# Kernel tuning notes

Hardware: AMD Instinct MI355X
Metric: run time of the kernel (lower is better)

## Reference

```python
import jax, jax.numpy as jnp
import numpy as np

NUM_HEADS = 32
NUM_KV_HEADS = 8
HEAD_DIM = 128
NEG_INF = -1e9


def rotate_half(x):
    x1, x2 = jnp.split(x, 2, axis=-1)
    return jnp.concatenate([-x2, x1], axis=-1)


def setup_inputs() -> dict:
    key = jax.random.key(0)
    ks = jax.random.split(key, 8)
    B, S, H = 2, 2048, 4096
    hidden_states = jax.random.normal(ks[0], (B, S, H), jnp.float32) * 0.02
    # additive causal mask [1,1,S,S]: 0 on/below diagonal, -1e9 above
    causal = jnp.tril(jnp.ones((S, S), bool))
    attention_mask = jnp.where(causal, 0.0, NEG_INF)[None, None, :, :].astype(jnp.float32)
    # RoPE tables (theta=500000 style), shape [1,S,head_dim]
    inv_freq = 1.0 / (500000.0 ** (np.arange(0, HEAD_DIM, 2, dtype=np.float32) / HEAD_DIM))
    t = np.arange(S, dtype=np.float32)
    freqs = np.outer(t, inv_freq)  # [S, head_dim/2]
    emb = np.concatenate([freqs, freqs], axis=-1)  # [S, head_dim]
    cos = jnp.asarray(np.cos(emb))[None]
    sin = jnp.asarray(np.sin(emb))[None]
    scale = 0.02
    wq = jax.random.normal(ks[1], (NUM_HEADS * HEAD_DIM, H), jnp.float32) * scale
    wk = jax.random.normal(ks[2], (NUM_KV_HEADS * HEAD_DIM, H), jnp.float32) * scale
    wv = jax.random.normal(ks[3], (NUM_KV_HEADS * HEAD_DIM, H), jnp.float32) * scale
    wo = jax.random.normal(ks[4], (H, NUM_HEADS * HEAD_DIM), jnp.float32) * scale
    return {"hidden_states": hidden_states, "attention_mask": attention_mask,
            "cos": cos, "sin": sin, "wq": wq, "wk": wk, "wv": wv, "wo": wo}


def reference(hidden_states, attention_mask, cos, sin, wq, wk, wv, wo):
    B, S, H = hidden_states.shape
    nh, nkv, hd = NUM_HEADS, NUM_KV_HEADS, HEAD_DIM
    groups = nh // nkv
    # QKV projections (bias=False)
    q = jnp.einsum('bsh,dh->bsd', hidden_states, wq).reshape(B, S, nh, hd).transpose(0, 2, 1, 3)
    k = jnp.einsum('bsh,dh->bsd', hidden_states, wk).reshape(B, S, nkv, hd).transpose(0, 2, 1, 3)
    v = jnp.einsum('bsh,dh->bsd', hidden_states, wv).reshape(B, S, nkv, hd).transpose(0, 2, 1, 3)
    # RoPE: cos/sin [1,S,hd] -> broadcast over head dim [1,1,S,hd]
    c = cos[:, None, :, :]
    s = sin[:, None, :, :]
    q = q * c + rotate_half(q) * s
    k = k * c + rotate_half(k) * s
    # GQA: repeat_kv
    k = jnp.repeat(k, groups, axis=1)  # [B,nh,S,hd]
    v = jnp.repeat(v, groups, axis=1)
    # SDPA with additive mask
    scores = jnp.einsum('bhqd,bhkd->bhqk', q, k) / jnp.sqrt(jnp.float32(hd))
    scores = scores + attention_mask[:, :, :, :k.shape[2]]
    attn = jax.nn.softmax(scores, axis=-1)
    out = jnp.einsum('bhqk,bhkd->bhqd', attn, v)  # [B,nh,S,hd]
    out = out.transpose(0, 2, 1, 3).reshape(B, S, nh * hd)
    return jnp.einsum('bsd,hd->bsh', out, wo)
```

## Files before the change

### kernel.cpp

```cpp
#include <hip/hip_runtime.h>
#include <hip/hip_bf16.h>

typedef __attribute__((ext_vector_type(8))) __bf16 bf16x8;
typedef __attribute__((ext_vector_type(4))) float f32x4;
typedef __attribute__((ext_vector_type(16))) float f32x16;
typedef __attribute__((ext_vector_type(4))) unsigned int u32x4;

#define SEQ 2048
#define NH 32
#define NKV 8
#define HD 128

__device__ __forceinline__ ushort f2bf(float f) {
  unsigned u = __builtin_bit_cast(unsigned, f);
  unsigned r = (u + 0x7fffu + ((u >> 16) & 1u)) >> 16;
  return (ushort)r;
}
__device__ __forceinline__ float bf2f(ushort h) {
  return __builtin_bit_cast(float, ((unsigned)h) << 16);
}
__device__ __forceinline__ unsigned cvt_pk_bf16(float lo, float hi) {
  unsigned r;
  asm("v_cvt_pk_bf16_f32 %0, %1, %2" : "=v"(r) : "v"(lo), "v"(hi));
  return r;
}
__device__ __forceinline__ void gload16(const void* g, void* l) {
  __builtin_amdgcn_global_load_lds(
      (const __attribute__((address_space(1))) void*)g,
      (__attribute__((address_space(3))) void*)l, 16, 0, 0);
}

__global__ __launch_bounds__(256) void f2bf_kernel(const float4* __restrict__ in,
                                                   ushort4* __restrict__ out, int n4) {
  int i = blockIdx.x * 256 + threadIdx.x;
  if (i >= n4) return;
  float4 v = in[i];
  ushort4 o;
  o.x = f2bf(v.x); o.y = f2bf(v.y); o.z = f2bf(v.z); o.w = f2bf(v.w);
  out[i] = o;
}

template <int OUTF32>
__global__ __launch_bounds__(256) void gemm_bt_kernel(const ushort* __restrict__ A,
                                                      const ushort* __restrict__ B,
                                                      void* __restrict__ C,
                                                      int M, int N, int K) {
  __shared__ ushort As[2][128 * 32];
  __shared__ ushort Bs[2][128 * 32];
  const int tid = threadIdx.x;
  const int w = tid >> 6, l = tid & 63;
  const int lr = l & 15, lc = l >> 4;
  const int bx = blockIdx.x, by = blockIdx.y;
  const int wr = w >> 1, wc = w & 1;

  f32x4 z = {0.f, 0.f, 0.f, 0.f};
  f32x4 acc[4][4];
#pragma unroll
  for (int i = 0; i < 4; ++i)
#pragma unroll
    for (int j = 0; j < 4; ++j) acc[i][j] = z;

  const ushort* aSrc = A + (size_t)(by * 128 + 32 * w + (l >> 2)) * K + (l & 3) * 8;
  const ushort* bSrc = B + (size_t)(bx * 128 + 32 * w + (l >> 2)) * K + (l & 3) * 8;
  const int ldsOff = (32 * w) * 32;

#pragma unroll
  for (int q = 0; q < 2; ++q) {
    gload16(aSrc + (size_t)q * 16 * K, &As[0][ldsOff + q * 512]);
    gload16(bSrc + (size_t)q * 16 * K, &Bs[0][ldsOff + q * 512]);
  }
  __syncthreads();

  const int nk = K >> 5;
  int cur = 0;
  for (int kt = 0; kt < nk; ++kt) {
    if (kt + 1 < nk) {
      const ushort* a2 = aSrc + (size_t)(kt + 1) * 32;
      const ushort* b2 = bSrc + (size_t)(kt + 1) * 32;
#pragma unroll
      for (int q = 0; q < 2; ++q) {
        gload16(a2 + (size_t)q * 16 * K, &As[cur ^ 1][ldsOff + q * 512]);
        gload16(b2 + (size_t)q * 16 * K, &Bs[cur ^ 1][ldsOff + q * 512]);
      }
    }
    bf16x8 af[4], bfr[4];
#pragma unroll
    for (int i = 0; i < 4; ++i)
      af[i] = *(const bf16x8*)&As[cur][(64 * wr + 16 * i + lr) * 32 + lc * 8];
#pragma unroll
    for (int j = 0; j < 4; ++j)
      bfr[j] = *(const bf16x8*)&Bs[cur][(64 * wc + 16 * j + lr) * 32 + lc * 8];
#pragma unroll
    for (int i = 0; i < 4; ++i)
#pragma unroll
      for (int j = 0; j < 4; ++j)
        acc[i][j] = __builtin_amdgcn_mfma_f32_16x16x32_bf16(af[i], bfr[j], acc[i][j], 0, 0, 0);
    __syncthreads();
    cur ^= 1;
  }

#pragma unroll
  for (int i = 0; i < 4; ++i)
#pragma unroll
    for (int j = 0; j < 4; ++j) {
      int row = by * 128 + 64 * wr + 16 * i + lc * 4;
      int col = bx * 128 + 64 * wc + 16 * j + lr;
#pragma unroll
      for (int r = 0; r < 4; ++r) {
        if (OUTF32)
          ((float*)C)[(size_t)(row + r) * N + col] = acc[i][j][r];
        else
          ((ushort*)C)[(size_t)(row + r) * N + col] = f2bf(acc[i][j][r]);
      }
    }
}

template <int OUTF32>
__global__ __launch_bounds__(512, 2) void gemm256_kernel(const ushort* __restrict__ A,
                                                         const ushort* __restrict__ B,
                                                         void* __restrict__ C,
                                                         int M, int N, int K) {
  __shared__ ushort As[2][256 * 64];
  __shared__ ushort Bs[2][256 * 64];
  const int tid = threadIdx.x;
  const int w = tid >> 6, l = tid & 63;
  const int lr = l & 15, lc = l >> 4;
  const int wr = w >> 2, wc = w & 3;

  const int nbx = N >> 8;
  const int cpx = gridDim.x >> 3;
  const int sw = (blockIdx.x & 7) * cpx + (blockIdx.x >> 3);
  const int bx = sw % nbx, by = sw / nbx;

  const ushort* Asrc = A + (size_t)(by * 256) * K;
  const ushort* Bsrc = B + (size_t)(bx * 256) * K;

  f32x4 z = {0.f, 0.f, 0.f, 0.f};
  f32x4 acc[8][4];
#pragma unroll
  for (int m = 0; m < 8; ++m)
#pragma unroll
    for (int n = 0; n < 4; ++n) acc[m][n] = z;

  const int NK = K >> 6;

  auto stage = [&](int kt2, int s) {
    if (kt2 >= NK) return;
    const int mat = s >> 1, half = s & 1;
    const ushort* g = mat ? Bsrc : Asrc;
    char* lb = (char*)(mat ? &Bs[kt2 & 1][0] : &As[kt2 & 1][0]) + half * 16384 + w * 1024;
#pragma unroll
    for (int i = 0; i < 2; ++i) {
      int row = half * 128 + i * 64 + w * 8 + (l >> 3);
      int csw = ((l & 7) * 16) ^ ((row & 7) << 4);
      gload16(g + (size_t)row * K + kt2 * 64 + (csw >> 1), lb + i * 8192);
    }
  };

  stage(0, 0); stage(0, 1); stage(0, 2); stage(0, 3);
  stage(1, 0);

  bf16x8 af[4][2], bfr[4][2];
  for (int kt = 0; kt < NK; ++kt) {
    const char* Ab = (const char*)&As[kt & 1][0];
    const char* Bb = (const char*)&Bs[kt & 1][0];
    if (kt + 1 < NK) asm volatile("s_waitcnt vmcnt(2)" ::: "memory");
    else             asm volatile("s_waitcnt vmcnt(0)" ::: "memory");
    asm volatile("s_barrier" ::: "memory");

#pragma unroll
    for (int m = 0; m < 4; ++m) {
      int row = wr * 128 + m * 16 + lr;
#pragma unroll
      for (int ks = 0; ks < 2; ++ks)
        af[m][ks] = *(const bf16x8*)(Ab + row * 128 + ((ks * 64 + lc * 16) ^ ((row & 7) << 4)));
    }
#pragma unroll
    for (int n = 0; n < 2; ++n) {
      int row = wc * 64 + n * 16 + lr;
#pragma unroll
      for (int ks = 0; ks < 2; ++ks)
        bfr[n][ks] = *(const bf16x8*)(Bb + row * 128 + ((ks * 64 + lc * 16) ^ ((row & 7) << 4)));
    }
    stage(kt + 1, 1);
    __builtin_amdgcn_s_setprio(1);
#pragma unroll
    for (int m = 0; m < 4; ++m)
#pragma unroll
      for (int n = 0; n < 2; ++n)
#pragma unroll
        for (int ks = 0; ks < 2; ++ks)
          acc[m][n] = __builtin_amdgcn_mfma_f32_16x16x32_bf16(af[m][ks], bfr[n][ks], acc[m][n], 0, 0, 0);
    __builtin_amdgcn_s_setprio(0);
    asm volatile("s_barrier" ::: "memory");

#pragma unroll
    for (int n = 2; n < 4; ++n) {
      int row = wc * 64 + n * 16 + lr;
#pragma unroll
      for (int ks = 0; ks < 2; ++ks)
        bfr[n][ks] = *(const bf16x8*)(Bb + row * 128 + ((ks * 64 + lc * 16) ^ ((row & 7) << 4)));
    }
    stage(kt + 1, 2);
    __builtin_amdgcn_s_setprio(1);
#pragma unroll
    for (int m = 0; m < 4; ++m)
#pragma unroll
      for (int n = 2; n < 4; ++n)
#pragma unroll
        for (int ks = 0; ks < 2; ++ks)
          acc[m][n] = __builtin_amdgcn_mfma_f32_16x16x32_bf16(af[m][ks], bfr[n][ks], acc[m][n], 0, 0, 0);
    __builtin_amdgcn_s_setprio(0);
    asm volatile("s_barrier" ::: "memory");

#pragma unroll
    for (int m = 0; m < 4; ++m) {
      int row = wr * 128 + (m + 4) * 16 + lr;
#pragma unroll
      for (int ks = 0; ks < 2; ++ks)
        af[m][ks] = *(const bf16x8*)(Ab + row * 128 + ((ks * 64 + lc * 16) ^ ((row & 7) << 4)));
    }
    stage(kt + 1, 3);
    __builtin_amdgcn_s_setprio(1);
#pragma unroll
    for (int m = 0; m < 4; ++m)
#pragma unroll
      for (int n = 0; n < 2; ++n)
#pragma unroll
        for (int ks = 0; ks < 2; ++ks)
          acc[m + 4][n] = __builtin_amdgcn_mfma_f32_16x16x32_bf16(af[m][ks], bfr[n][ks], acc[m + 4][n], 0, 0, 0);
    __builtin_amdgcn_s_setprio(0);
    asm volatile("s_barrier" ::: "memory");

    stage(kt + 2, 0);
    __builtin_amdgcn_s_setprio(1);
#pragma unroll
    for (int m = 0; m < 4; ++m)
#pragma unroll
      for (int n = 2; n < 4; ++n)
#pragma unroll
        for (int ks = 0; ks < 2; ++ks)
          acc[m + 4][n] = __builtin_amdgcn_mfma_f32_16x16x32_bf16(af[m][ks], bfr[n][ks], acc[m + 4][n], 0, 0, 0);
    __builtin_amdgcn_s_setprio(0);
  }

#pragma unroll
  for (int m = 0; m < 8; ++m)
#pragma unroll
    for (int n = 0; n < 4; ++n) {
      int row = by * 256 + wr * 128 + m * 16 + lc * 4;
      int col = bx * 256 + wc * 64 + n * 16 + lr;
#pragma unroll
      for (int r = 0; r < 4; ++r) {
        if (OUTF32)
          ((float*)C)[(size_t)(row + r) * N + col] = acc[m][n][r];
        else
          ((ushort*)C)[(size_t)(row + r) * N + col] = f2bf(acc[m][n][r]);
      }
    }
}

__global__ __launch_bounds__(256) void rope_kernel(const ushort* __restrict__ in,
                                                   const float* __restrict__ cosb,
                                                   const float* __restrict__ sinb,
                                                   ushort* __restrict__ out,
                                                   int hshift, float scale) {
  int idx = blockIdx.x * 256 + threadIdx.x;
  int d = idx & 63;
  int nh = 1 << hshift;
  int h = (idx >> 6) & (nh - 1);
  int rowg = idx >> (6 + hshift);
  int s = rowg & (SEQ - 1);
  int b = rowg >> 11;
  const ushort* p = in + (size_t)rowg * (nh * HD) + h * HD + d;
  float x = bf2f(p[0]), y = bf2f(p[64]);
  float c = cosb[s * HD + d], sn = sinb[s * HD + d];
  ushort* qo = out + (((size_t)(b * nh + h)) * SEQ + s) * HD + d;
  qo[0] = f2bf((x * c - y * sn) * scale);
  qo[64] = f2bf((y * c + x * sn) * scale);
}

__global__ __launch_bounds__(256) void vtrans_kernel(const ushort* __restrict__ vin,
                                                     ushort* __restrict__ vout) {
  __shared__ ushort t[64][66];
  const int s0 = blockIdx.x * 64;
  const int c0 = blockIdx.y * 64;
  const int b = blockIdx.z;
  const int tx = threadIdx.x & 63;
  const int ty = threadIdx.x >> 6;
#pragma unroll
  for (int rr = 0; rr < 64; rr += 4) {
    int r = rr + ty;
    t[r][tx] = vin[((size_t)(b * SEQ + s0 + r)) * (NKV * HD) + c0 + tx];
  }
  __syncthreads();
#pragma unroll
  for (int rr = 0; rr < 64; rr += 4) {
    int c = rr + ty;
    int cg = c0 + c;
    int kvh = cg >> 7, d = cg & 127;
    vout[(((size_t)(b * NKV + kvh)) * HD + d) * SEQ + s0 + tx] = t[tx][c];
  }
}

__global__ __launch_bounds__(256, 2) void attn_kernel(const ushort* __restrict__ Qh,
                                                      const ushort* __restrict__ Kh,
                                                      const ushort* __restrict__ Vt,
                                                      ushort* __restrict__ Out) {
  __shared__ ushort Kl[2][64 * 128];

  const int tid = threadIdx.x;
  const int w = tid >> 6, l = tid & 63;
  const int lq = l & 31;
  const int hl = l >> 5;

  const int n = blockIdx.x;
  const int m = ((n & 7) << 6) + (n >> 3);
  const int pp = m >> 5;
  const int rm = m & 31;
  const int h2 = rm >> 3;
  const int qpi = rm & 7;
  const int bb = pp >> 3, kvh = pp & 7;
  const int hh = kvh * 4 + h2;
  const int bh = bb * 32 + hh;

  const ushort* Kbase = Kh + ((size_t)(bb * NKV + kvh) * SEQ) * HD;
  const ushort* Vbase = Vt + ((size_t)(bb * NKV + kvh) * HD) * SEQ;

  auto stageK = [&](int buf, int t) {
    const int kv0 = t * 64;
#pragma unroll
    for (int q = 0; q < 4; ++q) {
      int chunk = 4 * w + q;
      int row = chunk * 4 + (l >> 4);
      int cs = ((l & 15) ^ (row & 7)) * 8;
      gload16(Kbase + ((size_t)(kv0 + row)) * HD + cs, &Kl[buf][chunk * 512]);
    }
  };

  for (int qsel = 0; qsel < 2; ++qsel) {
    const int qt = qsel ? (15 - qpi) : qpi;
    const int q0 = qt * 128;
    const int wrow0 = q0 + 32 * w;
    const int qrow = wrow0 + lq;

    bf16x8 qf[8];
    {
      const ushort* qrp = Qh + ((size_t)bh * SEQ + qrow) * HD + 8 * hl;
#pragma unroll
      for (int s8 = 0; s8 < 8; ++s8) qf[s8] = *(const bf16x8*)(qrp + 16 * s8);
    }

    f32x16 o[4];
#pragma unroll
    for (int db = 0; db < 4; ++db)
#pragma unroll
      for (int i = 0; i < 16; ++i) o[db][i] = 0.f;
    float m_run = -1e30f, l_run = 0.f;

    const int ntw = 2 * qt + (w >> 1) + 1;
    const int ntb = 2 * qt + 2;

    stageK(0, 0);
    __syncthreads();

    int cur = 0;
    for (int t = 0; t < ntb; ++t) {
      const int kv0 = t * 64;
      if (t + 1 < ntb) stageK(cur ^ 1, t + 1);

      if (t < ntw) {
        f32x16 sacc[2];
#pragma unroll
        for (int b2 = 0; b2 < 2; ++b2)
#pragma unroll
          for (int i = 0; i < 16; ++i) sacc[b2][i] = 0.f;

        const int swz = lq & 7;
        __builtin_amdgcn_s_setprio(1);
#pragma unroll
        for (int s8 = 0; s8 < 8; ++s8) {
#pragma unroll
          for (int b2 = 0; b2 < 2; ++b2) {
            int row = 32 * b2 + lq;
            bf16x8 kf = *(const bf16x8*)((const char*)&Kl[cur][0] + row * 256 +
                                         (((2 * s8 + hl) ^ swz) << 4));
            sacc[b2] = __builtin_amdgcn_mfma_f32_32x32x16_bf16(kf, qf[s8], sacc[b2], 0, 0, 0);
          }
        }
        __builtin_amdgcn_s_setprio(0);

        if (t == ntw - 1) {
#pragma unroll
          for (int b2 = 0; b2 < 2; ++b2)
#pragma unroll
            for (int r = 0; r < 16; ++r) {
              int kv = kv0 + 32 * b2 + (r & 3) + 8 * (r >> 2) + 4 * hl;
              if (kv > qrow) sacc[b2][r] = -1e30f;
            }
        }

        float mx = sacc[0][0];
#pragma unroll
        for (int r = 1; r < 16; ++r) mx = fmaxf(mx, sacc[0][r]);
#pragma unroll
        for (int r = 0; r < 16; ++r) mx = fmaxf(mx, sacc[1][r]);
        mx = fmaxf(mx, __shfl_xor(mx, 32));

        if (__any(mx > m_run + 8.0f)) {
          float mn = fmaxf(m_run, mx);
          float sc = __expf(m_run - mn);
          m_run = mn;
          l_run *= sc;
#pragma unroll
          for (int db = 0; db < 4; ++db) o[db] *= sc;
        }

        float sum = 0.f;
#pragma unroll
        for (int b2 = 0; b2 < 2; ++b2)
#pragma unroll
          for (int r = 0; r < 16; ++r) {
            float e = __expf(sacc[b2][r] - m_run);
            sacc[b2][r] = e;
            sum += e;
          }
        sum += __shfl_xor(sum, 32);
        l_run += sum;

        unsigned pw[2][8];
#pragma unroll
        for (int b2 = 0; b2 < 2; ++b2)
#pragma unroll
          for (int i = 0; i < 8; ++i)
            pw[b2][i] = cvt_pk_bf16(sacc[b2][2 * i], sacc[b2][2 * i + 1]);

#pragma unroll
        for (int s = 0; s < 4; ++s) {
          const int b2 = s >> 1, bs = 4 * (s & 1);
          unsigned wA = pw[b2][bs], wB = pw[b2][bs + 1], wC = pw[b2][bs + 2], wD = pw[b2][bs + 3];
          unsigned s1 = hl ? wA : wC, s2 = hl ? wB : wD;
          unsigned rx1 = (unsigned)__shfl_xor((int)s1, 32);
          unsigned rx2 = (unsigned)__shfl_xor((int)s2, 32);
          u32x4 fw = {hl ? rx1 : wA, hl ? rx2 : wB, hl ? wC : rx1, hl ? wD : rx2};
          bf16x8 pfrag = __builtin_bit_cast(bf16x8, fw);
          const ushort* vp = Vbase + (size_t)lq * SEQ + kv0 + 16 * s + 8 * hl;
          bf16x8 vf[4];
#pragma unroll
          for (int db = 0; db < 4; ++db) vf[db] = *(const bf16x8*)(vp + (size_t)(32 * db) * SEQ);
          __builtin_amdgcn_s_setprio(1);
#pragma unroll
          for (int db = 0; db < 4; ++db)
            o[db] = __builtin_amdgcn_mfma_f32_32x32x16_bf16(vf[db], pfrag, o[db], 0, 0, 0);
          __builtin_amdgcn_s_setprio(0);
        }
      }
      __syncthreads();
      cur ^= 1;
    }

    const float inv = 1.0f / l_run;
    ushort* outp = Out + ((size_t)bb * SEQ + qrow) * (NH * HD) + hh * HD;
#pragma unroll
    for (int db = 0; db < 4; ++db)
#pragma unroll
      for (int i = 0; i < 8; ++i) {
        unsigned wrd = cvt_pk_bf16(o[db][2 * i] * inv, o[db][2 * i + 1] * inv);
        int d = 32 * db + 2 * (i & 1) + 8 * (i >> 1) + 4 * hl;
        *(unsigned*)(outp + d) = wrd;
      }
  }
}

extern "C" void kernel_launch(void* const* d_in, const int* in_sizes, int n_in,
                              void* d_out, int out_size, void* d_ws, size_t ws_size,
                              hipStream_t stream) {
  const float* hs = (const float*)d_in[0];
  const float* cosb = (const float*)d_in[2];
  const float* sinb = (const float*)d_in[3];
  const float* wq = (const float*)d_in[4];
  const float* wk = (const float*)d_in[5];
  const float* wv = (const float*)d_in[6];
  const float* wo = (const float*)d_in[7];

  char* ws = (char*)d_ws;
  ushort* hs_bf = (ushort*)(ws);
  ushort* wq_bf = (ushort*)(ws + 33554432);
  ushort* wk_bf = (ushort*)(ws + 67108864);
  ushort* wv_bf = (ushort*)(ws + 75497472);
  ushort* wo_bf = (ushort*)(ws + 83886080);
  ushort* q_lin = (ushort*)(ws + 117440512);
  ushort* k_lin = (ushort*)(ws + 150994944);
  ushort* v_lin = (ushort*)(ws + 159383552);
  ushort* Qh = hs_bf;
  ushort* Kh = wq_bf;
  ushort* Vt = (ushort*)(ws + 41943040);
  ushort* attn_out = q_lin;

  f2bf_kernel<<<16384, 256, 0, stream>>>((const float4*)hs, (ushort4*)hs_bf, 4194304);
  f2bf_kernel<<<16384, 256, 0, stream>>>((const float4*)wq, (ushort4*)wq_bf, 4194304);
  f2bf_kernel<<<4096, 256, 0, stream>>>((const float4*)wk, (ushort4*)wk_bf, 1048576);
  f2bf_kernel<<<4096, 256, 0, stream>>>((const float4*)wv, (ushort4*)wv_bf, 1048576);
  f2bf_kernel<<<16384, 256, 0, stream>>>((const float4*)wo, (ushort4*)wo_bf, 4194304);

  gemm256_kernel<0><<<256, 512, 0, stream>>>(hs_bf, wq_bf, q_lin, 4096, 4096, 4096);
  gemm_bt_kernel<0><<<dim3(8, 32), 256, 0, stream>>>(hs_bf, wk_bf, k_lin, 4096, 1024, 4096);
  gemm_bt_kernel<0><<<dim3(8, 32), 256, 0, stream>>>(hs_bf, wv_bf, v_lin, 4096, 1024, 4096);

  rope_kernel<<<32768, 256, 0, stream>>>(q_lin, cosb, sinb, Qh, 5, 0.08838834764831845f);
  rope_kernel<<<8192, 256, 0, stream>>>(k_lin, cosb, sinb, Kh, 3, 1.0f);
  vtrans_kernel<<<dim3(32, 16, 2), 256, 0, stream>>>(v_lin, Vt);

  attn_kernel<<<512, 256, 0, stream>>>(Qh, Kh, Vt, attn_out);

  gemm256_kernel<1><<<256, 512, 0, stream>>>(attn_out, wo_bf, d_out, 4096, 4096, 4096);
}
```

Measured before the change: 622.3 us.

## Split attention into per-q-tile blocks, fuse K/V GEMM, use exp2 softmax

The attention kernel now gives each block a single 128-row query tile, heaviest tiles first, and launches 1024 blocks instead of 512 blocks that each processed two paired tiles. Occupancy is raised to 4 blocks per CU via launch bounds. The K and V projections become one GEMM over the contiguous wk/wv weights, writing into a single interleaved buffer that rope and the V transpose read with a new stride. Softmax uses the raw v_exp_f32 (base 2) with log2(e) folded into the Q scale, and the max and sum reductions become tree reductions. The higher occupancy target caps registers per thread and risks spills, and per-block Q loads and K staging setup are now repeated more often.

```diff
diff --git a/kernel.cpp b/kernel.cpp
--- a/kernel.cpp
+++ b/kernel.cpp
@@ -22,6 +22,11 @@
 __device__ __forceinline__ unsigned cvt_pk_bf16(float lo, float hi) {
   unsigned r;
   asm("v_cvt_pk_bf16_f32 %0, %1, %2" : "=v"(r) : "v"(lo), "v"(hi));
+  return r;
+}
+__device__ __forceinline__ float exp2_fast(float x) {
+  float r;
+  asm("v_exp_f32 %0, %1" : "=v"(r) : "v"(x));
   return r;
 }
 __device__ __forceinline__ void gload16(const void* g, void* l) {
@@ -260,7 +265,7 @@
     }
 }
 
-__global__ __launch_bounds__(256) void rope_kernel(const ushort* __restrict__ in,
+__global__ __launch_bounds__(256) void rope_kernel(const ushort* __restrict__ in, int ld,
                                                    const float* __restrict__ cosb,
                                                    const float* __restrict__ sinb,
                                                    ushort* __restrict__ out,
@@ -272,7 +277,7 @@
   int rowg = idx >> (6 + hshift);
   int s = rowg & (SEQ - 1);
   int b = rowg >> 11;
-  const ushort* p = in + (size_t)rowg * (nh * HD) + h * HD + d;
+  const ushort* p = in + (size_t)rowg * ld + h * HD + d;
   float x = bf2f(p[0]), y = bf2f(p[64]);
   float c = cosb[s * HD + d], sn = sinb[s * HD + d];
   ushort* qo = out + (((size_t)(b * nh + h)) * SEQ + s) * HD + d;
@@ -291,7 +296,7 @@
 #pragma unroll
   for (int rr = 0; rr < 64; rr += 4) {
     int r = rr + ty;
-    t[r][tx] = vin[((size_t)(b * SEQ + s0 + r)) * (NKV * HD) + c0 + tx];
+    t[r][tx] = vin[((size_t)(b * SEQ + s0 + r)) * 2048 + 1024 + c0 + tx];
   }
   __syncthreads();
 #pragma unroll
@@ -303,7 +308,7 @@
   }
 }
 
-__global__ __launch_bounds__(256, 2) void attn_kernel(const ushort* __restrict__ Qh,
+__global__ __launch_bounds__(256, 4) void attn_kernel(const ushort* __restrict__ Qh,
                                                       const ushort* __restrict__ Kh,
                                                       const ushort* __restrict__ Vt,
                                                       ushort* __restrict__ Out) {
@@ -315,17 +320,37 @@
   const int hl = l >> 5;
 
   const int n = blockIdx.x;
-  const int m = ((n & 7) << 6) + (n >> 3);
-  const int pp = m >> 5;
-  const int rm = m & 31;
-  const int h2 = rm >> 3;
-  const int qpi = rm & 7;
+  const int xcd = n & 7, i = n >> 3;
+  const int qt = 15 - (i >> 3);
+  const int j = i & 7;
+  const int pp = 2 * xcd + (j >> 2);
+  const int h2 = j & 3;
   const int bb = pp >> 3, kvh = pp & 7;
   const int hh = kvh * 4 + h2;
   const int bh = bb * 32 + hh;
+  const int q0 = qt * 128;
+  const int wrow0 = q0 + 32 * w;
+  const int qrow = wrow0 + lq;
 
   const ushort* Kbase = Kh + ((size_t)(bb * NKV + kvh) * SEQ) * HD;
   const ushort* Vbase = Vt + ((size_t)(bb * NKV + kvh) * HD) * SEQ;
+
+  bf16x8 qf[8];
+  {
+    const ushort* qrp = Qh + ((size_t)bh * SEQ + qrow) * HD + 8 * hl;
+#pragma unroll
+    for (int s8 = 0; s8 < 8; ++s8) qf[s8] = *(const bf16x8*)(qrp + 16 * s8);
+  }
+
+  f32x16 o[4];
+#pragma unroll
+  for (int db = 0; db < 4; ++db)
+#pragma unroll
+    for (int i2 = 0; i2 < 16; ++i2) o[db][i2] = 0.f;
+  float m_run = -1e30f, l_run = 0.f;
+
+  const int ntw = 2 * qt + (w >> 1) + 1;
+  const int ntb = 2 * qt + 2;
 
   auto stageK = [&](int buf, int t) {
     const int kv0 = t * 64;
@@ -338,138 +363,120 @@
     }
   };
 
-  for (int qsel = 0; qsel < 2; ++qsel) {
-    const int qt = qsel ? (15 - qpi) : qpi;
-    const int q0 = qt * 128;
-    const int wrow0 = q0 + 32 * w;
-    const int qrow = wrow0 + lq;
-
-    bf16x8 qf[8];
-    {
-      const ushort* qrp = Qh + ((size_t)bh * SEQ + qrow) * HD + 8 * hl;
-#pragma unroll
-      for (int s8 = 0; s8 < 8; ++s8) qf[s8] = *(const bf16x8*)(qrp + 16 * s8);
-    }
-
-    f32x16 o[4];
-#pragma unroll
-    for (int db = 0; db < 4; ++db)
-#pragma unroll
-      for (int i = 0; i < 16; ++i) o[db][i] = 0.f;
-    float m_run = -1e30f, l_run = 0.f;
-
-    const int ntw = 2 * qt + (w >> 1) + 1;
-    const int ntb = 2 * qt + 2;
-
-    stageK(0, 0);
+  stageK(0, 0);
+  __syncthreads();
+
+  int cur = 0;
+  for (int t = 0; t < ntb; ++t) {
+    const int kv0 = t * 64;
+    if (t + 1 < ntb) stageK(cur ^ 1, t + 1);
+
+    if (t < ntw) {
+      f32x16 sacc[2];
+#pragma unroll
+      for (int b2 = 0; b2 < 2; ++b2)
+#pragma unroll
+        for (int i2 = 0; i2 < 16; ++i2) sacc[b2][i2] = 0.f;
+
+      const int swz = lq & 7;
+      __builtin_amdgcn_s_setprio(1);
+#pragma unroll
+      for (int s8 = 0; s8 < 8; ++s8) {
+#pragma unroll
+        for (int b2 = 0; b2 < 2; ++b2) {
+          int row = 32 * b2 + lq;
+          bf16x8 kf = *(const bf16x8*)((const char*)&Kl[cur][0] + row * 256 +
+                                       (((2 * s8 + hl) ^ swz) << 4));
+          sacc[b2] = __builtin_amdgcn_mfma_f32_32x32x16_bf16(kf, qf[s8], sacc[b2], 0, 0, 0);
+        }
+      }
+      __builtin_amdgcn_s_setprio(0);
+
+      if (t == ntw - 1) {
+#pragma unroll
+        for (int b2 = 0; b2 < 2; ++b2)
+#pragma unroll
+          for (int r = 0; r < 16; ++r) {
+            int kv = kv0 + 32 * b2 + (r & 3) + 8 * (r >> 2) + 4 * hl;
+            if (kv > qrow) sacc[b2][r] = -1e30f;
+          }
+      }
+
+      float tm[8];
+#pragma unroll
+      for (int r = 0; r < 8; ++r)
+        tm[r] = fmaxf(fmaxf(sacc[0][r], sacc[0][r + 8]),
+                      fmaxf(sacc[1][r], sacc[1][r + 8]));
+#pragma unroll
+      for (int s2 = 4; s2; s2 >>= 1)
+#pragma unroll
+        for (int r = 0; r < s2; ++r) tm[r] = fmaxf(tm[r], tm[r + s2]);
+      float mx = fmaxf(tm[0], __shfl_xor(tm[0], 32));
+
+      if (__any(mx > m_run + 8.0f)) {
+        float mn = fmaxf(m_run, mx);
+        float sc = exp2_fast(m_run - mn);
+        m_run = mn;
+        l_run *= sc;
+#pragma unroll
+        for (int db = 0; db < 4; ++db) o[db] *= sc;
+      }
+
+#pragma unroll
+      for (int b2 = 0; b2 < 2; ++b2)
+#pragma unroll
+        for (int r = 0; r < 16; ++r) sacc[b2][r] = exp2_fast(sacc[b2][r] - m_run);
+      float ts[8];
+#pragma unroll
+      for (int r = 0; r < 8; ++r)
+        ts[r] = (sacc[0][r] + sacc[0][r + 8]) + (sacc[1][r] + sacc[1][r + 8]);
+#pragma unroll
+      for (int s2 = 4; s2; s2 >>= 1)
+#pragma unroll
+        for (int r = 0; r < s2; ++r) ts[r] += ts[r + s2];
+      l_run += ts[0] + __shfl_xor(ts[0], 32);
+
+      unsigned pw[2][8];
+#pragma unroll
+      for (int b2 = 0; b2 < 2; ++b2)
+#pragma unroll
+        for (int i2 = 0; i2 < 8; ++i2)
+          pw[b2][i2] = cvt_pk_bf16(sacc[b2][2 * i2], sacc[b2][2 * i2 + 1]);
+
+#pragma unroll
+      for (int s = 0; s < 4; ++s) {
+        const int b2 = s >> 1, bs = 4 * (s & 1);
+        unsigned wA = pw[b2][bs], wB = pw[b2][bs + 1], wC = pw[b2][bs + 2], wD = pw[b2][bs + 3];
+        unsigned s1 = hl ? wA : wC, s2v = hl ? wB : wD;
+        unsigned rx1 = (unsigned)__shfl_xor((int)s1, 32);
+        unsigned rx2 = (unsigned)__shfl_xor((int)s2v, 32);
+        u32x4 fw = {hl ? rx1 : wA, hl ? rx2 : wB, hl ? wC : rx1, hl ? wD : rx2};
+        bf16x8 pfrag = __builtin_bit_cast(bf16x8, fw);
+        const ushort* vp = Vbase + (size_t)lq * SEQ + kv0 + 16 * s + 8 * hl;
+        bf16x8 vf[4];
+#pragma unroll
+        for (int db = 0; db < 4; ++db) vf[db] = *(const bf16x8*)(vp + (size_t)(32 * db) * SEQ);
+        __builtin_amdgcn_s_setprio(1);
+#pragma unroll
+        for (int db = 0; db < 4; ++db)
+          o[db] = __builtin_amdgcn_mfma_f32_32x32x16_bf16(vf[db], pfrag, o[db], 0, 0, 0);
+        __builtin_amdgcn_s_setprio(0);
+      }
+    }
     __syncthreads();
-
-    int cur = 0;
-    for (int t = 0; t < ntb; ++t) {
-      const int kv0 = t * 64;
-      if (t + 1 < ntb) stageK(cur ^ 1, t + 1);
-
-      if (t < ntw) {
-        f32x16 sacc[2];
-#pragma unroll
-        for (int b2 = 0; b2 < 2; ++b2)
-#pragma unroll
-          for (int i = 0; i < 16; ++i) sacc[b2][i] = 0.f;
-
-        const int swz = lq & 7;
-        __builtin_amdgcn_s_setprio(1);
-#pragma unroll
-        for (int s8 = 0; s8 < 8; ++s8) {
-#pragma unroll
-          for (int b2 = 0; b2 < 2; ++b2) {
-            int row = 32 * b2 + lq;
-            bf16x8 kf = *(const bf16x8*)((const char*)&Kl[cur][0] + row * 256 +
-                                         (((2 * s8 + hl) ^ swz) << 4));
-            sacc[b2] = __builtin_amdgcn_mfma_f32_32x32x16_bf16(kf, qf[s8], sacc[b2], 0, 0, 0);
-          }
-        }
-        __builtin_amdgcn_s_setprio(0);
-
-        if (t == ntw - 1) {
-#pragma unroll
-          for (int b2 = 0; b2 < 2; ++b2)
-#pragma unroll
-            for (int r = 0; r < 16; ++r) {
-              int kv = kv0 + 32 * b2 + (r & 3) + 8 * (r >> 2) + 4 * hl;
-              if (kv > qrow) sacc[b2][r] = -1e30f;
-            }
-        }
-
-        float mx = sacc[0][0];
-#pragma unroll
-        for (int r = 1; r < 16; ++r) mx = fmaxf(mx, sacc[0][r]);
-#pragma unroll
-        for (int r = 0; r < 16; ++r) mx = fmaxf(mx, sacc[1][r]);
-        mx = fmaxf(mx, __shfl_xor(mx, 32));
-
-        if (__any(mx > m_run + 8.0f)) {
-          float mn = fmaxf(m_run, mx);
-          float sc = __expf(m_run - mn);
-          m_run = mn;
-          l_run *= sc;
-#pragma unroll
-          for (int db = 0; db < 4; ++db) o[db] *= sc;
-        }
-
-        float sum = 0.f;
-#pragma unroll
-        for (int b2 = 0; b2 < 2; ++b2)
-#pragma unroll
-          for (int r = 0; r < 16; ++r) {
-            float e = __expf(sacc[b2][r] - m_run);
-            sacc[b2][r] = e;
-            sum += e;
-          }
-        sum += __shfl_xor(sum, 32);
-        l_run += sum;
-
-        unsigned pw[2][8];
-#pragma unroll
-        for (int b2 = 0; b2 < 2; ++b2)
-#pragma unroll
-          for (int i = 0; i < 8; ++i)
-            pw[b2][i] = cvt_pk_bf16(sacc[b2][2 * i], sacc[b2][2 * i + 1]);
-
-#pragma unroll
-        for (int s = 0; s < 4; ++s) {
-          const int b2 = s >> 1, bs = 4 * (s & 1);
-          unsigned wA = pw[b2][bs], wB = pw[b2][bs + 1], wC = pw[b2][bs + 2], wD = pw[b2][bs + 3];
-          unsigned s1 = hl ? wA : wC, s2 = hl ? wB : wD;
-          unsigned rx1 = (unsigned)__shfl_xor((int)s1, 32);
-          unsigned rx2 = (unsigned)__shfl_xor((int)s2, 32);
-          u32x4 fw = {hl ? rx1 : wA, hl ? rx2 : wB, hl ? wC : rx1, hl ? wD : rx2};
-          bf16x8 pfrag = __builtin_bit_cast(bf16x8, fw);
-          const ushort* vp = Vbase + (size_t)lq * SEQ + kv0 + 16 * s + 8 * hl;
-          bf16x8 vf[4];
-#pragma unroll
-          for (int db = 0; db < 4; ++db) vf[db] = *(const bf16x8*)(vp + (size_t)(32 * db) * SEQ);
-          __builtin_amdgcn_s_setprio(1);
-#pragma unroll
-          for (int db = 0; db < 4; ++db)
-            o[db] = __builtin_amdgcn_mfma_f32_32x32x16_bf16(vf[db], pfrag, o[db], 0, 0, 0);
-          __builtin_amdgcn_s_setprio(0);
-        }
-      }
-      __syncthreads();
-      cur ^= 1;
-    }
-
-    const float inv = 1.0f / l_run;
-    ushort* outp = Out + ((size_t)bb * SEQ + qrow) * (NH * HD) + hh * HD;
-#pragma unroll
-    for (int db = 0; db < 4; ++db)
-#pragma unroll
-      for (int i = 0; i < 8; ++i) {
-        unsigned wrd = cvt_pk_bf16(o[db][2 * i] * inv, o[db][2 * i + 1] * inv);
-        int d = 32 * db + 2 * (i & 1) + 8 * (i >> 1) + 4 * hl;
-        *(unsigned*)(outp + d) = wrd;
-      }
-  }
+    cur ^= 1;
+  }
+
+  const float inv = 1.0f / l_run;
+  ushort* outp = Out + ((size_t)bb * SEQ + qrow) * (NH * HD) + hh * HD;
+#pragma unroll
+  for (int db = 0; db < 4; ++db)
+#pragma unroll
+    for (int i2 = 0; i2 < 8; ++i2) {
+      unsigned wrd = cvt_pk_bf16(o[db][2 * i2] * inv, o[db][2 * i2 + 1] * inv);
+      int d = 32 * db + 2 * (i2 & 1) + 8 * (i2 >> 1) + 4 * hl;
+      *(unsigned*)(outp + d) = wrd;
+    }
 }
 
 extern "C" void kernel_launch(void* const* d_in, const int* in_sizes, int n_in,
@@ -490,8 +497,7 @@
   ushort* wv_bf = (ushort*)(ws + 75497472);
   ushort* wo_bf = (ushort*)(ws + 83886080);
   ushort* q_lin = (ushort*)(ws + 117440512);
-  ushort* k_lin = (ushort*)(ws + 150994944);
-  ushort* v_lin = (ushort*)(ws + 159383552);
+  ushort* kv_lin = (ushort*)(ws + 150994944);
   ushort* Qh = hs_bf;
   ushort* Kh = wq_bf;
   ushort* Vt = (ushort*)(ws + 41943040);
@@ -504,14 +510,14 @@
   f2bf_kernel<<<16384, 256, 0, stream>>>((const float4*)wo, (ushort4*)wo_bf, 4194304);
 
   gemm256_kernel<0><<<256, 512, 0, stream>>>(hs_bf, wq_bf, q_lin, 4096, 4096, 4096);
-  gemm_bt_kernel<0><<<dim3(8, 32), 256, 0, stream>>>(hs_bf, wk_bf, k_lin, 4096, 1024, 4096);
-  gemm_bt_kernel<0><<<dim3(8, 32), 256, 0, stream>>>(hs_bf, wv_bf, v_lin, 4096, 1024, 4096);
-
-  rope_kernel<<<32768, 256, 0, stream>>>(q_lin, cosb, sinb, Qh, 5, 0.08838834764831845f);
-  rope_kernel<<<8192, 256, 0, stream>>>(k_lin, cosb, sinb, Kh, 3, 1.0f);
-  vtrans_kernel<<<dim3(32, 16, 2), 256, 0, stream>>>(v_lin, Vt);
-
-  attn_kernel<<<512, 256, 0, stream>>>(Qh, Kh, Vt, attn_out);
+  gemm_bt_kernel<0><<<dim3(16, 32), 256, 0, stream>>>(hs_bf, wk_bf, kv_lin, 4096, 2048, 4096);
+
+  rope_kernel<<<32768, 256, 0, stream>>>(q_lin, 4096, cosb, sinb, Qh, 5,
+                                         0.08838834764831845f * 1.4426950408889634f);
+  rope_kernel<<<8192, 256, 0, stream>>>(kv_lin, 2048, cosb, sinb, Kh, 3, 1.0f);
+  vtrans_kernel<<<dim3(32, 16, 2), 256, 0, stream>>>(kv_lin, Vt);
+
+  attn_kernel<<<1024, 256, 0, stream>>>(Qh, Kh, Vt, attn_out);
 
   gemm256_kernel<1><<<256, 512, 0, stream>>>(attn_out, wo_bf, d_out, 4096, 4096, 4096);
 }
```

New measurement: 708.3 us. 13.8% more time.
